# Kernel optimization log

Hardware: AMD Instinct MI355X
Metric: run time of the kernel (lower is better)

Reference implementation:

```python
import jax, jax.numpy as jnp
import numpy as np
import math

H = 16          # num_attention_heads
D = 64          # attention_head_size
MAX_POS = 1024  # max_position_embeddings


def setup_inputs() -> dict:
    key = jax.random.key(0)
    ks = jax.random.split(key, 6)
    B, S, HID = 4, 1024, 1024
    scale = 1.0 / math.sqrt(HID)
    return {
        "hidden_states": jax.random.normal(ks[0], (B, S, HID), jnp.float32),
        "attention_mask": jnp.zeros((B, 1, 1, S), jnp.float32),
        "Wq": jax.random.normal(ks[1], (HID, HID), jnp.float32) * scale,
        "bq": jnp.zeros((HID,), jnp.float32),
        "Wk": jax.random.normal(ks[2], (HID, HID), jnp.float32) * scale,
        "bk": jnp.zeros((HID,), jnp.float32),
        "Wv": jax.random.normal(ks[3], (HID, HID), jnp.float32) * scale,
        "bv": jnp.zeros((HID,), jnp.float32),
        "dist_emb": jax.random.normal(ks[4], (2 * MAX_POS - 1, D), jnp.float32) * 0.02,
    }


def _split_heads(x):
    # [B,S,H*D] -> [B,H,S,D]
    B, S, _ = x.shape
    return x.reshape(B, S, H, D).transpose(0, 2, 1, 3)


def reference(hidden_states, attention_mask, Wq, bq, Wk, bk, Wv, bv, dist_emb):
    B, S, _ = hidden_states.shape
    q = _split_heads(hidden_states @ Wq.T + bq)   # [B,H,S,D]
    k = _split_heads(hidden_states @ Wk.T + bk)
    v = _split_heads(hidden_states @ Wv.T + bv)

    scores = jnp.einsum("bhqd,bhkd->bhqk", q, k)  # [B,H,S,S]

    # relative_key_query positional bias
    pos_l = jnp.arange(S)[:, None]
    pos_r = jnp.arange(S)[None, :]
    distance = pos_l - pos_r + (MAX_POS - 1)      # [S,S] in [0, 2*MAX_POS-2]
    pos_emb = dist_emb[distance]                  # [S,S,D]
    rel_q = jnp.einsum("bhld,lrd->bhlr", q, pos_emb)
    rel_k = jnp.einsum("bhrd,lrd->bhlr", k, pos_emb)
    scores = (scores + rel_q + rel_k) / math.sqrt(D)

    scores = scores + attention_mask
    probs = jax.nn.softmax(scores, axis=-1)
    ctx = jnp.einsum("bhqk,bhkd->bhqd", probs, v)  # [B,H,S,D]
    ctx = ctx.transpose(0, 2, 1, 3).reshape(B, S, H * D)
    return ctx
```

## Files before the change

### kernel.cpp

```cpp
#include <hip/hip_runtime.h>
#include <hip/hip_bf16.h>

#define B_   4
#define S_   1024
#define HID_ 1024
#define H_   16
#define D_   64

typedef __attribute__((ext_vector_type(4))) float f32x4;
typedef __attribute__((ext_vector_type(8))) __bf16 bf16v8;
typedef __attribute__((ext_vector_type(8))) unsigned short u16x8;

#define MFMA16(a, b, c) __builtin_amdgcn_mfma_f32_16x16x32_bf16((a), (b), (c), 0, 0, 0)
#define GLOAD16(gp, lp)                                                              \
    __builtin_amdgcn_global_load_lds((const __attribute__((address_space(1))) void*)(gp), \
                                     (__attribute__((address_space(3))) void*)(lp), 16, 0, 0)

__device__ __forceinline__ unsigned short f2bs_hw(float f) {
    __bf16 h = (__bf16)f;
    return __builtin_bit_cast(unsigned short, h);
}
__device__ __forceinline__ unsigned pack2bf(float a, float b) {
    unsigned short lo = f2bs_hw(a), hi = f2bs_hw(b);
    return (unsigned)lo | ((unsigned)hi << 16);
}
__device__ __forceinline__ float bs2f(unsigned short s) {
    union { unsigned u; float f; } v; v.u = ((unsigned)s) << 16;
    return v.f;
}

__global__ void conv_kernel(const float* __restrict__ src, unsigned short* __restrict__ dst,
                            int n4) {
    int i = blockIdx.x * 256 + threadIdx.x;
    int stride = gridDim.x * 256;
    for (; i < n4; i += stride) {
        float4 x = *(const float4*)(src + (size_t)i * 4);
        uint2 o;
        o.x = pack2bf(x.x, x.y);
        o.y = pack2bf(x.z, x.w);
        *(uint2*)(dst + (size_t)i * 4) = o;
    }
}

__global__ __launch_bounds__(256)
void proj_kernel(const unsigned short* __restrict__ Xb,
                 const unsigned short* __restrict__ Wqb, const float* __restrict__ bq,
                 const unsigned short* __restrict__ Wkb, const float* __restrict__ bk,
                 const unsigned short* __restrict__ Wvb, const float* __restrict__ bv,
                 unsigned short* __restrict__ Qo, unsigned short* __restrict__ Ko,
                 unsigned short* __restrict__ Vo)
{
    __shared__ __align__(16) unsigned short Al[128][64];
    __shared__ __align__(16) unsigned short Bl[128][64];

    const int bid = blockIdx.x;
    const int tile = (bid & 7) * 96 + (bid >> 3);
    const int rt = tile / 24, ct = tile % 24;
    const int row0 = rt * 128, col0 = ct * 128;
    const int which = col0 >> 10;
    const unsigned short* Wm = (which == 0) ? Wqb : (which == 1) ? Wkb : Wvb;
    const float* bias        = (which == 0) ? bq  : (which == 1) ? bk  : bv;
    unsigned short* Out      = (which == 0) ? Qo  : (which == 1) ? Ko  : Vo;
    const int oc0 = col0 & 1023;

    const int t = threadIdx.x;
    const int lane = t & 63, w = t >> 6;
    const int wr = w >> 1, wc = w & 1;
    const int lg = lane >> 4, lc = lane & 15;

    f32x4 acc[4][4] = {};

    for (int k0 = 0; k0 < 1024; k0 += 64) {
        __syncthreads();
#pragma unroll
        for (int l = 0; l < 4; ++l) {
            int idx = l * 256 + t;
            int r = idx >> 3, su = idx & 7;
            int u = su ^ (r & 7);
            GLOAD16(Xb + (size_t)(row0 + r) * 1024 + k0 + u * 8,
                    &Al[0][0] + (size_t)(l * 256 + w * 64) * 8);
            GLOAD16(Wm + (size_t)(oc0 + r) * 1024 + k0 + u * 8,
                    &Bl[0][0] + (size_t)(l * 256 + w * 64) * 8);
        }
        __syncthreads();

        bf16v8 af[4][2], bfg[4][2];
#pragma unroll
        for (int m = 0; m < 4; ++m)
#pragma unroll
            for (int ks = 0; ks < 2; ++ks) {
                int u = (ks * 4 + lg) ^ (lc & 7);
                af[m][ks] = *(const bf16v8*)&Al[wr * 64 + m * 16 + lc][u * 8];
            }
#pragma unroll
        for (int n = 0; n < 4; ++n)
#pragma unroll
            for (int ks = 0; ks < 2; ++ks) {
                int u = (ks * 4 + lg) ^ (lc & 7);
                bfg[n][ks] = *(const bf16v8*)&Bl[wc * 64 + n * 16 + lc][u * 8];
            }
        __builtin_amdgcn_s_setprio(1);
#pragma unroll
        for (int m = 0; m < 4; ++m)
#pragma unroll
            for (int n = 0; n < 4; ++n) {
                acc[m][n] = MFMA16(af[m][0], bfg[n][0], acc[m][n]);
                acc[m][n] = MFMA16(af[m][1], bfg[n][1], acc[m][n]);
            }
        __builtin_amdgcn_s_setprio(0);
    }

#pragma unroll
    for (int m = 0; m < 4; ++m)
#pragma unroll
        for (int n = 0; n < 4; ++n) {
            int j = oc0 + wc * 64 + n * 16 + lc;
            int hh = j >> 6, dd = j & 63;
            float bv_ = bias[j];
#pragma unroll
            for (int r = 0; r < 4; ++r) {
                int i = row0 + wr * 64 + m * 16 + lg * 4 + r;
                int bb = i >> 10, ss = i & 1023;
                float v = acc[m][n][r] + bv_;
                Out[((size_t)(bb * 16 + hh) * 1024 + ss) * 64 + dd] = f2bs_hw(v);
            }
        }
}

__global__ __launch_bounds__(256)
void attn_kernel(const unsigned short* __restrict__ Q,
                 const unsigned short* __restrict__ K,
                 const unsigned short* __restrict__ V,
                 const float* __restrict__ mask,
                 const unsigned short* __restrict__ Eb,
                 float* __restrict__ Out)
{
    __shared__ __align__(16) unsigned short Kl[64][64];
    __shared__ __align__(16) unsigned short El[128][64];
    __shared__ __align__(16) unsigned short VTl[64][72];
    __shared__ __align__(16) unsigned short QDl[4][16][136];
    __shared__ __align__(16) unsigned short KDl[64][132];
    __shared__ __align__(16) unsigned Pex[4 * 16 * 36];
    __shared__ float maskl[64];

    const int t = threadIdx.x;
    const int lane = t & 63, w = t >> 6;
    const int lg = lane >> 4, lc = lane & 15;

    const int bid = blockIdx.x;
    const int bh = bid & 63;
    const int qt = bid >> 6;
    const int b = bh >> 4, h = bh & 15;
    const int i0 = qt * 64;
    const int i_loc = w * 16 + lc;

    const float C2 = 0.125f * 1.44269504089f;
    const float L2E = 1.44269504089f;

    const unsigned short* Qh = Q + (size_t)bh * S_ * D_;
    const unsigned short* Kh = K + (size_t)bh * S_ * D_;
    const unsigned short* Vh = V + (size_t)bh * S_ * D_;

    bf16v8 qf[2];
#pragma unroll
    for (int ks = 0; ks < 2; ++ks)
        qf[ks] = *(const bf16v8*)(Qh + (size_t)(i0 + i_loc) * D_ + ks * 32 + lg * 8);

    u16x8 ones_u;
#pragma unroll
    for (int e = 0; e < 8; ++e) ones_u[e] = 0x3F80;
    const bf16v8 onesf = __builtin_bit_cast(bf16v8, ones_u);

    float m_r = -1e30f;
    f32x4 lacc = (f32x4){0.f, 0.f, 0.f, 0.f};
    f32x4 ctx[4];
#pragma unroll
    for (int nd = 0; nd < 4; ++nd) ctx[nd] = (f32x4){0.f, 0.f, 0.f, 0.f};

    unsigned* PexW = &Pex[(w * 16 + lc) * 36];

    for (int jt = 0; jt < 16; ++jt) {
        const int j0 = jt * 64;
        const int dbase = i0 - j0 + 960;
        __syncthreads();

#pragma unroll
        for (int l = 0; l < 2; ++l) {
            int idx = l * 256 + t;
            int r = idx >> 3, su = idx & 7;
            int u = su ^ (r & 7);
            GLOAD16(Kh + (size_t)(j0 + r) * 64 + u * 8,
                    &Kl[0][0] + (size_t)(l * 256 + w * 64) * 8);
        }
        {
            int a = t & 7, rb = (t >> 3) << 1;
            int cq = a * 8;
            u16x8 v0 = *(const u16x8*)(Vh + (size_t)(j0 + rb) * 64 + cq);
            u16x8 v1 = *(const u16x8*)(Vh + (size_t)(j0 + rb + 1) * 64 + cq);
            int jst = (rb + (a << 3)) & 63;
#pragma unroll
            for (int e = 0; e < 8; ++e)
                *(unsigned*)&VTl[cq + e][jst] = (unsigned)v0[e] | ((unsigned)v1[e] << 16);
        }
        if (jt == 0) {
            const int sb0 = dbase & 127;
#pragma unroll
            for (int l = 0; l < 4; ++l) {
                int idx = l * 256 + t;
                int sl = idx >> 3, su = idx & 7;
                int u = su ^ (sl & 7);
                int dr = dbase + ((sl - sb0) & 127);
                if (dr > 2046) dr = 2046;
                GLOAD16(Eb + (size_t)dr * 64 + u * 8,
                        &El[0][0] + (size_t)(l * 256 + w * 64) * 8);
            }
        } else {
            const int sb = dbase & 127;
#pragma unroll
            for (int l = 0; l < 2; ++l) {
                int idx = l * 256 + t;
                int rl = idx >> 3, su = idx & 7;
                int u = su ^ (rl & 7);
                GLOAD16(Eb + (size_t)(dbase + rl) * 64 + u * 8,
                        &El[sb][0] + (size_t)(l * 256 + w * 64) * 8);
            }
        }
        if (t < 64) maskl[t] = mask[(size_t)b * S_ + j0 + t] * L2E;
        __syncthreads();

        bf16v8 kfa[2];
#pragma unroll
        for (int ks = 0; ks < 2; ++ks) {
            int u = (ks * 4 + lg) ^ (lc & 7);
            kfa[ks] = *(const bf16v8*)&Kl[w * 16 + lc][u * 8];
        }
        __builtin_amdgcn_s_setprio(1);
#pragma unroll
        for (int nd = 0; nd < 8; ++nd) {
            int sl = (dbase + nd * 16 + lc) & 127;
            int u0 = lg ^ (lc & 7);
            int u1 = (4 + lg) ^ (lc & 7);
            bf16v8 ef0 = *(const bf16v8*)&El[sl][u0 * 8];
            bf16v8 ef1 = *(const bf16v8*)&El[sl][u1 * 8];
            f32x4 kd = (f32x4){0.f, 0.f, 0.f, 0.f};
            kd = MFMA16(ef0, kfa[0], kd);
            kd = MFMA16(ef1, kfa[1], kd);
            uint2 pk;
            pk.x = pack2bf(kd[0], kd[1]);
            pk.y = pack2bf(kd[2], kd[3]);
            *(uint2*)&KDl[w * 16 + lc][nd * 16 + lg * 4] = pk;
            if (nd < 4 || jt == 0) {
                f32x4 qd = (f32x4){0.f, 0.f, 0.f, 0.f};
                qd = MFMA16(ef0, qf[0], qd);
                qd = MFMA16(ef1, qf[1], qd);
                int slot0 = ((dbase & 127) + nd * 16 + lg * 4) & 127;
                uint2 qk2;
                qk2.x = pack2bf(qd[0], qd[1]);
                qk2.y = pack2bf(qd[2], qd[3]);
                *(uint2*)&QDl[w][lc][slot0] = qk2;
            }
        }
        __builtin_amdgcn_s_setprio(0);
        __syncthreads();

        f32x4 s[4];
#pragma unroll
        for (int n = 0; n < 4; ++n) {
            s[n] = (f32x4){0.f, 0.f, 0.f, 0.f};
#pragma unroll
            for (int ks = 0; ks < 2; ++ks) {
                int u = (ks * 4 + lg) ^ (lc & 7);
                bf16v8 kb = *(const bf16v8*)&Kl[n * 16 + lc][u * 8];
                s[n] = MFMA16(kb, qf[ks], s[n]);
            }
        }

        const unsigned short* QDw = &QDl[w][lc][0];
        float vmax = -1e30f;
#pragma unroll
        for (int n = 0; n < 4; ++n) {
            int jb = n * 16 + lg * 4;
            float4 mk = *(const float4*)&maskl[jb];
            int kbase = jb * 131 + i_loc + 63;
            int qbase = dbase + i_loc - jb + 63;
#pragma unroll
            for (int r = 0; r < 4; ++r) {
                float qdv = bs2f(QDw[(qbase - r) & 127]);
                float kdv = bs2f((&KDl[0][0])[kbase + 131 * r]);
                float mkr = (r == 0) ? mk.x : (r == 1) ? mk.y : (r == 2) ? mk.z : mk.w;
                float val = (s[n][r] + qdv + kdv) * C2 + mkr;
                s[n][r] = val;
                vmax = fmaxf(vmax, val);
            }
        }
        vmax = fmaxf(vmax, __shfl_xor(vmax, 16));
        vmax = fmaxf(vmax, __shfl_xor(vmax, 32));

        if (__any(vmax > m_r)) {
            float mnew = fmaxf(m_r, vmax);
            float alpha = exp2f(m_r - mnew);
            m_r = mnew;
#pragma unroll
            for (int r = 0; r < 4; ++r) lacc[r] *= alpha;
#pragma unroll
            for (int nd = 0; nd < 4; ++nd)
#pragma unroll
                for (int r = 0; r < 4; ++r)
                    ctx[nd][r] *= alpha;
        }

#pragma unroll
        for (int n = 0; n < 4; ++n)
#pragma unroll
            for (int r = 0; r < 4; ++r)
                s[n][r] = exp2f(s[n][r] - m_r);

#pragma unroll
        for (int n = 0; n < 4; ++n) {
            uint2 pk;
            pk.x = pack2bf(s[n][0], s[n][1]);
            pk.y = pack2bf(s[n][2], s[n][3]);
            *(uint2*)&PexW[n * 8 + lg * 2] = pk;
        }
        bf16v8 pfB[2];
#pragma unroll
        for (int ks = 0; ks < 2; ++ks) {
            int nc = 2 * ks + (lg >> 1);
            pfB[ks] = *(const bf16v8*)&PexW[nc * 8 + (lg & 1) * 4];
        }

        __builtin_amdgcn_s_setprio(1);
        lacc = MFMA16(onesf, pfB[0], lacc);
        lacc = MFMA16(onesf, pfB[1], lacc);
#pragma unroll
        for (int nd = 0; nd < 4; ++nd) {
            int vrow = nd * 16 + lc;
#pragma unroll
            for (int ks = 0; ks < 2; ++ks) {
                int jst = (ks * 32 + lg * 8 + ((vrow >> 3) << 3)) & 63;
                bf16v8 vf = *(const bf16v8*)&VTl[vrow][jst];
                ctx[nd] = MFMA16(vf, pfB[ks], ctx[nd]);
            }
        }
        __builtin_amdgcn_s_setprio(0);
    }

    float inv = 1.0f / lacc[0];
    float* outp = Out + ((size_t)(b * S_ + i0 + i_loc) * H_ + h) * D_;
#pragma unroll
    for (int nd = 0; nd < 4; ++nd) {
        float4 o;
        o.x = ctx[nd][0] * inv;
        o.y = ctx[nd][1] * inv;
        o.z = ctx[nd][2] * inv;
        o.w = ctx[nd][3] * inv;
        *(float4*)(outp + nd * 16 + lg * 4) = o;
    }
}

extern "C" void kernel_launch(void* const* d_in, const int* in_sizes, int n_in,
                              void* d_out, int out_size, void* d_ws, size_t ws_size,
                              hipStream_t stream)
{
    const float* X    = (const float*)d_in[0];
    const float* mask = (const float*)d_in[1];
    const float* Wq   = (const float*)d_in[2];
    const float* bq   = (const float*)d_in[3];
    const float* Wk   = (const float*)d_in[4];
    const float* bk   = (const float*)d_in[5];
    const float* Wv   = (const float*)d_in[6];
    const float* bv   = (const float*)d_in[7];
    const float* E    = (const float*)d_in[8];
    float* Out = (float*)d_out;

    const size_t headN = (size_t)B_ * H_ * S_ * D_;
    unsigned short* Qw  = (unsigned short*)d_ws;
    unsigned short* Kw  = Qw + headN;
    unsigned short* Vw  = Kw + headN;
    unsigned short* Ebw = Vw + headN;
    unsigned short* Xb  = Ebw + (size_t)2047 * 64;
    unsigned short* Wqb = Xb + (size_t)4096 * 1024;
    unsigned short* Wkb = Wqb + (size_t)1024 * 1024;
    unsigned short* Wvb = Wkb + (size_t)1024 * 1024;

    conv_kernel<<<dim3(128),  dim3(256), 0, stream>>>(E,  Ebw, 2047 * 64 / 4);
    conv_kernel<<<dim3(2048), dim3(256), 0, stream>>>(X,  Xb,  4096 * 1024 / 4);
    conv_kernel<<<dim3(1024), dim3(256), 0, stream>>>(Wq, Wqb, 1024 * 1024 / 4);
    conv_kernel<<<dim3(1024), dim3(256), 0, stream>>>(Wk, Wkb, 1024 * 1024 / 4);
    conv_kernel<<<dim3(1024), dim3(256), 0, stream>>>(Wv, Wvb, 1024 * 1024 / 4);
    proj_kernel<<<dim3(768), dim3(256), 0, stream>>>(Xb, Wqb, bq, Wkb, bk, Wvb, bv, Qw, Kw, Vw);
    attn_kernel<<<dim3(1024), dim3(256), 0, stream>>>(Qw, Kw, Vw, mask, Ebw, Out);
}
```

Measured before the change: 167.6 us.

## Double-buffer projection GEMM, prefetch attention tiles, merge conversion launches

The projection GEMM now double-buffers its LDS tiles, so the next K-slice's global-to-LDS loads are issued while MFMAs run on the current slice, and one barrier per iteration is removed. The attention kernel prefetches the next K/E tiles, V registers and mask values after the score MFMAs, and computes the full QD bias each iteration into a per-row layout with simpler indexing. The four weight/embedding conversions are merged into one launch, and the X conversion uses one element per thread. The costs are twice the projection LDS, more attention registers, and extra QD MFMA work on every iteration.

```diff
diff --git a/kernel.cpp b/kernel.cpp
--- a/kernel.cpp
+++ b/kernel.cpp
@@ -32,8 +32,29 @@
 __global__ void conv_kernel(const float* __restrict__ src, unsigned short* __restrict__ dst,
                             int n4) {
     int i = blockIdx.x * 256 + threadIdx.x;
-    int stride = gridDim.x * 256;
-    for (; i < n4; i += stride) {
+    if (i < n4) {
+        float4 x = *(const float4*)(src + (size_t)i * 4);
+        uint2 o;
+        o.x = pack2bf(x.x, x.y);
+        o.y = pack2bf(x.z, x.w);
+        *(uint2*)(dst + (size_t)i * 4) = o;
+    }
+}
+
+__global__ void conv4_kernel(const float* __restrict__ Wq, const float* __restrict__ Wk,
+                             const float* __restrict__ Wv, const float* __restrict__ E,
+                             unsigned short* __restrict__ Wqb, unsigned short* __restrict__ Wkb,
+                             unsigned short* __restrict__ Wvb, unsigned short* __restrict__ Eb) {
+    int bid = blockIdx.x;
+    const float* src;
+    unsigned short* dst;
+    int n4, base;
+    if (bid < 1024)      { src = Wq; dst = Wqb; n4 = 262144; base = bid; }
+    else if (bid < 2048) { src = Wk; dst = Wkb; n4 = 262144; base = bid - 1024; }
+    else if (bid < 3072) { src = Wv; dst = Wvb; n4 = 262144; base = bid - 2048; }
+    else                 { src = E;  dst = Eb;  n4 = 32752;  base = bid - 3072; }
+    int i = base * 256 + threadIdx.x;
+    if (i < n4) {
         float4 x = *(const float4*)(src + (size_t)i * 4);
         uint2 o;
         o.x = pack2bf(x.x, x.y);
@@ -50,8 +71,8 @@
                  unsigned short* __restrict__ Qo, unsigned short* __restrict__ Ko,
                  unsigned short* __restrict__ Vo)
 {
-    __shared__ __align__(16) unsigned short Al[128][64];
-    __shared__ __align__(16) unsigned short Bl[128][64];
+    __shared__ __align__(16) unsigned short Al[2][128][64];
+    __shared__ __align__(16) unsigned short Bl[2][128][64];
 
     const int bid = blockIdx.x;
     const int tile = (bid & 7) * 96 + (bid >> 3);
@@ -70,34 +91,47 @@
 
     f32x4 acc[4][4] = {};
 
-    for (int k0 = 0; k0 < 1024; k0 += 64) {
+#pragma unroll
+    for (int l = 0; l < 4; ++l) {
+        int idx = l * 256 + t;
+        int r = idx >> 3, su = idx & 7;
+        int u = su ^ (r & 7);
+        GLOAD16(Xb + (size_t)(row0 + r) * 1024 + u * 8,
+                &Al[0][0][0] + (size_t)(l * 256 + w * 64) * 8);
+        GLOAD16(Wm + (size_t)(oc0 + r) * 1024 + u * 8,
+                &Bl[0][0][0] + (size_t)(l * 256 + w * 64) * 8);
+    }
+
+    for (int it = 0; it < 16; ++it) {
+        const int p = it & 1;
         __syncthreads();
-#pragma unroll
-        for (int l = 0; l < 4; ++l) {
-            int idx = l * 256 + t;
-            int r = idx >> 3, su = idx & 7;
-            int u = su ^ (r & 7);
-            GLOAD16(Xb + (size_t)(row0 + r) * 1024 + k0 + u * 8,
-                    &Al[0][0] + (size_t)(l * 256 + w * 64) * 8);
-            GLOAD16(Wm + (size_t)(oc0 + r) * 1024 + k0 + u * 8,
-                    &Bl[0][0] + (size_t)(l * 256 + w * 64) * 8);
-        }
-        __syncthreads();
-
+        if (it < 15) {
+            const int k1 = (it + 1) * 64;
+#pragma unroll
+            for (int l = 0; l < 4; ++l) {
+                int idx = l * 256 + t;
+                int r = idx >> 3, su = idx & 7;
+                int u = su ^ (r & 7);
+                GLOAD16(Xb + (size_t)(row0 + r) * 1024 + k1 + u * 8,
+                        &Al[p ^ 1][0][0] + (size_t)(l * 256 + w * 64) * 8);
+                GLOAD16(Wm + (size_t)(oc0 + r) * 1024 + k1 + u * 8,
+                        &Bl[p ^ 1][0][0] + (size_t)(l * 256 + w * 64) * 8);
+            }
+        }
         bf16v8 af[4][2], bfg[4][2];
 #pragma unroll
         for (int m = 0; m < 4; ++m)
 #pragma unroll
             for (int ks = 0; ks < 2; ++ks) {
                 int u = (ks * 4 + lg) ^ (lc & 7);
-                af[m][ks] = *(const bf16v8*)&Al[wr * 64 + m * 16 + lc][u * 8];
+                af[m][ks] = *(const bf16v8*)&Al[p][wr * 64 + m * 16 + lc][u * 8];
             }
 #pragma unroll
         for (int n = 0; n < 4; ++n)
 #pragma unroll
             for (int ks = 0; ks < 2; ++ks) {
                 int u = (ks * 4 + lg) ^ (lc & 7);
-                bfg[n][ks] = *(const bf16v8*)&Bl[wc * 64 + n * 16 + lc][u * 8];
+                bfg[n][ks] = *(const bf16v8*)&Bl[p][wc * 64 + n * 16 + lc][u * 8];
             }
         __builtin_amdgcn_s_setprio(1);
 #pragma unroll
@@ -138,8 +172,8 @@
     __shared__ __align__(16) unsigned short Kl[64][64];
     __shared__ __align__(16) unsigned short El[128][64];
     __shared__ __align__(16) unsigned short VTl[64][72];
-    __shared__ __align__(16) unsigned short QDl[4][16][136];
-    __shared__ __align__(16) unsigned short KDl[64][132];
+    __shared__ __align__(16) unsigned short QDl[64][134];
+    __shared__ __align__(16) unsigned short KDl[64][134];
     __shared__ __align__(16) unsigned Pex[4 * 16 * 36];
     __shared__ float maskl[64];
 
@@ -179,53 +213,50 @@
 
     unsigned* PexW = &Pex[(w * 16 + lc) * 36];
 
-    for (int jt = 0; jt < 16; ++jt) {
-        const int j0 = jt * 64;
-        const int dbase = i0 - j0 + 960;
-        __syncthreads();
-
+    const unsigned short* KD0 = &KDl[0][0] + lg * 4 * 133 + i_loc + 63;
+    const unsigned short* QD0 = &QDl[0][0] + i_loc * 135 + 12 - lg * 4;
+
+    const int va = t & 7, vrb = (t >> 3) << 1;
+    const int vcq = va * 8;
+    const int vjst = (vrb + (va << 3)) & 63;
+
+    u16x8 v0c, v1c;
+    float mkc;
+    {
 #pragma unroll
         for (int l = 0; l < 2; ++l) {
             int idx = l * 256 + t;
             int r = idx >> 3, su = idx & 7;
             int u = su ^ (r & 7);
-            GLOAD16(Kh + (size_t)(j0 + r) * 64 + u * 8,
+            GLOAD16(Kh + (size_t)r * 64 + u * 8,
                     &Kl[0][0] + (size_t)(l * 256 + w * 64) * 8);
         }
-        {
-            int a = t & 7, rb = (t >> 3) << 1;
-            int cq = a * 8;
-            u16x8 v0 = *(const u16x8*)(Vh + (size_t)(j0 + rb) * 64 + cq);
-            u16x8 v1 = *(const u16x8*)(Vh + (size_t)(j0 + rb + 1) * 64 + cq);
-            int jst = (rb + (a << 3)) & 63;
-#pragma unroll
-            for (int e = 0; e < 8; ++e)
-                *(unsigned*)&VTl[cq + e][jst] = (unsigned)v0[e] | ((unsigned)v1[e] << 16);
-        }
-        if (jt == 0) {
-            const int sb0 = dbase & 127;
-#pragma unroll
-            for (int l = 0; l < 4; ++l) {
-                int idx = l * 256 + t;
-                int sl = idx >> 3, su = idx & 7;
-                int u = su ^ (sl & 7);
-                int dr = dbase + ((sl - sb0) & 127);
-                if (dr > 2046) dr = 2046;
-                GLOAD16(Eb + (size_t)dr * 64 + u * 8,
-                        &El[0][0] + (size_t)(l * 256 + w * 64) * 8);
-            }
-        } else {
-            const int sb = dbase & 127;
-#pragma unroll
-            for (int l = 0; l < 2; ++l) {
-                int idx = l * 256 + t;
-                int rl = idx >> 3, su = idx & 7;
-                int u = su ^ (rl & 7);
-                GLOAD16(Eb + (size_t)(dbase + rl) * 64 + u * 8,
-                        &El[sb][0] + (size_t)(l * 256 + w * 64) * 8);
-            }
-        }
-        if (t < 64) maskl[t] = mask[(size_t)b * S_ + j0 + t] * L2E;
+        const int db0 = i0 + 960;
+        const int sb0 = db0 & 127;
+#pragma unroll
+        for (int l = 0; l < 4; ++l) {
+            int idx = l * 256 + t;
+            int sl = idx >> 3, su = idx & 7;
+            int u = su ^ (sl & 7);
+            int dr = db0 + ((sl - sb0) & 127);
+            if (dr > 2046) dr = 2046;
+            GLOAD16(Eb + (size_t)dr * 64 + u * 8,
+                    &El[0][0] + (size_t)(l * 256 + w * 64) * 8);
+        }
+        v0c = *(const u16x8*)(Vh + (size_t)vrb * 64 + vcq);
+        v1c = *(const u16x8*)(Vh + (size_t)(vrb + 1) * 64 + vcq);
+        mkc = (t < 64) ? mask[(size_t)b * S_ + t] * L2E : 0.f;
+    }
+
+    for (int jt = 0; jt < 16; ++jt) {
+        const int j0 = jt * 64;
+        const int dbase = i0 - j0 + 960;
+
+        __syncthreads();
+#pragma unroll
+        for (int e = 0; e < 8; ++e)
+            *(unsigned*)&VTl[vcq + e][vjst] = (unsigned)v0c[e] | ((unsigned)v1c[e] << 16);
+        if (t < 64) maskl[t] = mkc;
         __syncthreads();
 
         bf16v8 kfa[2];
@@ -234,10 +265,11 @@
             int u = (ks * 4 + lg) ^ (lc & 7);
             kfa[ks] = *(const bf16v8*)&Kl[w * 16 + lc][u * 8];
         }
+        const int slb = dbase + lc;
         __builtin_amdgcn_s_setprio(1);
 #pragma unroll
         for (int nd = 0; nd < 8; ++nd) {
-            int sl = (dbase + nd * 16 + lc) & 127;
+            int sl = (slb + nd * 16) & 127;
             int u0 = lg ^ (lc & 7);
             int u1 = (4 + lg) ^ (lc & 7);
             bf16v8 ef0 = *(const bf16v8*)&El[sl][u0 * 8];
@@ -249,20 +281,14 @@
             pk.x = pack2bf(kd[0], kd[1]);
             pk.y = pack2bf(kd[2], kd[3]);
             *(uint2*)&KDl[w * 16 + lc][nd * 16 + lg * 4] = pk;
-            if (nd < 4 || jt == 0) {
-                f32x4 qd = (f32x4){0.f, 0.f, 0.f, 0.f};
-                qd = MFMA16(ef0, qf[0], qd);
-                qd = MFMA16(ef1, qf[1], qd);
-                int slot0 = ((dbase & 127) + nd * 16 + lg * 4) & 127;
-                uint2 qk2;
-                qk2.x = pack2bf(qd[0], qd[1]);
-                qk2.y = pack2bf(qd[2], qd[3]);
-                *(uint2*)&QDl[w][lc][slot0] = qk2;
-            }
-        }
-        __builtin_amdgcn_s_setprio(0);
-        __syncthreads();
-
+            f32x4 qd = (f32x4){0.f, 0.f, 0.f, 0.f};
+            qd = MFMA16(ef0, qf[0], qd);
+            qd = MFMA16(ef1, qf[1], qd);
+            uint2 qk2;
+            qk2.x = pack2bf(qd[0], qd[1]);
+            qk2.y = pack2bf(qd[2], qd[3]);
+            *(uint2*)&QDl[w * 16 + lc][nd * 16 + lg * 4] = qk2;
+        }
         f32x4 s[4];
 #pragma unroll
         for (int n = 0; n < 4; ++n) {
@@ -274,20 +300,43 @@
                 s[n] = MFMA16(kb, qf[ks], s[n]);
             }
         }
-
-        const unsigned short* QDw = &QDl[w][lc][0];
+        __builtin_amdgcn_s_setprio(0);
+        __syncthreads();
+
+        if (jt < 15) {
+            const int j0n = j0 + 64;
+            const int dbn = dbase - 64;
+            const int sbn = dbn & 127;
+#pragma unroll
+            for (int l = 0; l < 2; ++l) {
+                int idx = l * 256 + t;
+                int r = idx >> 3, su = idx & 7;
+                int u = su ^ (r & 7);
+                GLOAD16(Kh + (size_t)(j0n + r) * 64 + u * 8,
+                        &Kl[0][0] + (size_t)(l * 256 + w * 64) * 8);
+            }
+#pragma unroll
+            for (int l = 0; l < 2; ++l) {
+                int idx = l * 256 + t;
+                int rl = idx >> 3, su = idx & 7;
+                int u = su ^ (rl & 7);
+                GLOAD16(Eb + (size_t)(dbn + rl) * 64 + u * 8,
+                        &El[sbn][0] + (size_t)(l * 256 + w * 64) * 8);
+            }
+            v0c = *(const u16x8*)(Vh + (size_t)(j0n + vrb) * 64 + vcq);
+            v1c = *(const u16x8*)(Vh + (size_t)(j0n + vrb + 1) * 64 + vcq);
+            mkc = (t < 64) ? mask[(size_t)b * S_ + j0n + t] * L2E : 0.f;
+        }
+
         float vmax = -1e30f;
 #pragma unroll
         for (int n = 0; n < 4; ++n) {
-            int jb = n * 16 + lg * 4;
-            float4 mk = *(const float4*)&maskl[jb];
-            int kbase = jb * 131 + i_loc + 63;
-            int qbase = dbase + i_loc - jb + 63;
+            float4 mk4 = *(const float4*)&maskl[n * 16 + lg * 4];
 #pragma unroll
             for (int r = 0; r < 4; ++r) {
-                float qdv = bs2f(QDw[(qbase - r) & 127]);
-                float kdv = bs2f((&KDl[0][0])[kbase + 131 * r]);
-                float mkr = (r == 0) ? mk.x : (r == 1) ? mk.y : (r == 2) ? mk.z : mk.w;
+                float qdv = bs2f(QD0[51 - 16 * n - r]);
+                float kdv = bs2f(KD0[133 * (16 * n + r)]);
+                float mkr = (r == 0) ? mk4.x : (r == 1) ? mk4.y : (r == 2) ? mk4.z : mk4.w;
                 float val = (s[n][r] + qdv + kdv) * C2 + mkr;
                 s[n][r] = val;
                 vmax = fmaxf(vmax, val);
@@ -383,11 +432,8 @@
     unsigned short* Wkb = Wqb + (size_t)1024 * 1024;
     unsigned short* Wvb = Wkb + (size_t)1024 * 1024;
 
-    conv_kernel<<<dim3(128),  dim3(256), 0, stream>>>(E,  Ebw, 2047 * 64 / 4);
-    conv_kernel<<<dim3(2048), dim3(256), 0, stream>>>(X,  Xb,  4096 * 1024 / 4);
-    conv_kernel<<<dim3(1024), dim3(256), 0, stream>>>(Wq, Wqb, 1024 * 1024 / 4);
-    conv_kernel<<<dim3(1024), dim3(256), 0, stream>>>(Wk, Wkb, 1024 * 1024 / 4);
-    conv_kernel<<<dim3(1024), dim3(256), 0, stream>>>(Wv, Wvb, 1024 * 1024 / 4);
+    conv_kernel<<<dim3(4096), dim3(256), 0, stream>>>(X, Xb, 4096 * 1024 / 4);
+    conv4_kernel<<<dim3(3200), dim3(256), 0, stream>>>(Wq, Wk, Wv, E, Wqb, Wkb, Wvb, Ebw);
     proj_kernel<<<dim3(768), dim3(256), 0, stream>>>(Xb, Wqb, bq, Wkb, bk, Wvb, bv, Qw, Kw, Vw);
     attn_kernel<<<dim3(1024), dim3(256), 0, stream>>>(Qw, Kw, Vw, mask, Ebw, Out);
 }
```

After: 173.5 us. 1.04x slower.

## Double-buffer projection GEMM tiles, merge conversion launches, move attn barrier

Applied to the files above, without the earlier changes.

The projection GEMM now double-buffers its LDS tiles, prefetching the next K-slice with global_load_lds while computing the current one, which removes one barrier per iteration. The four small weight/embedding conversion launches are merged into one kernel, and the X conversion uses one element per thread with no grid-stride loop. In the attention kernel a barrier and priority reset are moved after the QK score MFMAs so those overlap with other waves. The double buffer doubles LDS use in proj_kernel, which may lower occupancy.

```diff
diff --git a/kernel.cpp b/kernel.cpp
--- a/kernel.cpp
+++ b/kernel.cpp
@@ -10,6 +10,7 @@
 typedef __attribute__((ext_vector_type(4))) float f32x4;
 typedef __attribute__((ext_vector_type(8))) __bf16 bf16v8;
 typedef __attribute__((ext_vector_type(8))) unsigned short u16x8;
+typedef __attribute__((ext_vector_type(4))) unsigned short u16x4;
 
 #define MFMA16(a, b, c) __builtin_amdgcn_mfma_f32_16x16x32_bf16((a), (b), (c), 0, 0, 0)
 #define GLOAD16(gp, lp)                                                              \
@@ -32,8 +33,29 @@
 __global__ void conv_kernel(const float* __restrict__ src, unsigned short* __restrict__ dst,
                             int n4) {
     int i = blockIdx.x * 256 + threadIdx.x;
-    int stride = gridDim.x * 256;
-    for (; i < n4; i += stride) {
+    if (i < n4) {
+        float4 x = *(const float4*)(src + (size_t)i * 4);
+        uint2 o;
+        o.x = pack2bf(x.x, x.y);
+        o.y = pack2bf(x.z, x.w);
+        *(uint2*)(dst + (size_t)i * 4) = o;
+    }
+}
+
+__global__ void conv4_kernel(const float* __restrict__ Wq, const float* __restrict__ Wk,
+                             const float* __restrict__ Wv, const float* __restrict__ E,
+                             unsigned short* __restrict__ Wqb, unsigned short* __restrict__ Wkb,
+                             unsigned short* __restrict__ Wvb, unsigned short* __restrict__ Eb) {
+    int bid = blockIdx.x;
+    const float* src;
+    unsigned short* dst;
+    int n4, base;
+    if (bid < 1024)      { src = Wq; dst = Wqb; n4 = 262144; base = bid; }
+    else if (bid < 2048) { src = Wk; dst = Wkb; n4 = 262144; base = bid - 1024; }
+    else if (bid < 3072) { src = Wv; dst = Wvb; n4 = 262144; base = bid - 2048; }
+    else                 { src = E;  dst = Eb;  n4 = 32752;  base = bid - 3072; }
+    int i = base * 256 + threadIdx.x;
+    if (i < n4) {
         float4 x = *(const float4*)(src + (size_t)i * 4);
         uint2 o;
         o.x = pack2bf(x.x, x.y);
@@ -50,8 +72,8 @@
                  unsigned short* __restrict__ Qo, unsigned short* __restrict__ Ko,
                  unsigned short* __restrict__ Vo)
 {
-    __shared__ __align__(16) unsigned short Al[128][64];
-    __shared__ __align__(16) unsigned short Bl[128][64];
+    __shared__ __align__(16) unsigned short Al[2][128][64];
+    __shared__ __align__(16) unsigned short Bl[2][128][64];
 
     const int bid = blockIdx.x;
     const int tile = (bid & 7) * 96 + (bid >> 3);
@@ -70,34 +92,47 @@
 
     f32x4 acc[4][4] = {};
 
-    for (int k0 = 0; k0 < 1024; k0 += 64) {
+#pragma unroll
+    for (int l = 0; l < 4; ++l) {
+        int idx = l * 256 + t;
+        int r = idx >> 3, su = idx & 7;
+        int u = su ^ (r & 7);
+        GLOAD16(Xb + (size_t)(row0 + r) * 1024 + u * 8,
+                &Al[0][0][0] + (size_t)(l * 256 + w * 64) * 8);
+        GLOAD16(Wm + (size_t)(oc0 + r) * 1024 + u * 8,
+                &Bl[0][0][0] + (size_t)(l * 256 + w * 64) * 8);
+    }
+
+    for (int it = 0; it < 16; ++it) {
+        const int p = it & 1;
         __syncthreads();
-#pragma unroll
-        for (int l = 0; l < 4; ++l) {
-            int idx = l * 256 + t;
-            int r = idx >> 3, su = idx & 7;
-            int u = su ^ (r & 7);
-            GLOAD16(Xb + (size_t)(row0 + r) * 1024 + k0 + u * 8,
-                    &Al[0][0] + (size_t)(l * 256 + w * 64) * 8);
-            GLOAD16(Wm + (size_t)(oc0 + r) * 1024 + k0 + u * 8,
-                    &Bl[0][0] + (size_t)(l * 256 + w * 64) * 8);
-        }
-        __syncthreads();
-
+        if (it < 15) {
+            const int k1 = (it + 1) * 64;
+#pragma unroll
+            for (int l = 0; l < 4; ++l) {
+                int idx = l * 256 + t;
+                int r = idx >> 3, su = idx & 7;
+                int u = su ^ (r & 7);
+                GLOAD16(Xb + (size_t)(row0 + r) * 1024 + k1 + u * 8,
+                        &Al[p ^ 1][0][0] + (size_t)(l * 256 + w * 64) * 8);
+                GLOAD16(Wm + (size_t)(oc0 + r) * 1024 + k1 + u * 8,
+                        &Bl[p ^ 1][0][0] + (size_t)(l * 256 + w * 64) * 8);
+            }
+        }
         bf16v8 af[4][2], bfg[4][2];
 #pragma unroll
         for (int m = 0; m < 4; ++m)
 #pragma unroll
             for (int ks = 0; ks < 2; ++ks) {
                 int u = (ks * 4 + lg) ^ (lc & 7);
-                af[m][ks] = *(const bf16v8*)&Al[wr * 64 + m * 16 + lc][u * 8];
+                af[m][ks] = *(const bf16v8*)&Al[p][wr * 64 + m * 16 + lc][u * 8];
             }
 #pragma unroll
         for (int n = 0; n < 4; ++n)
 #pragma unroll
             for (int ks = 0; ks < 2; ++ks) {
                 int u = (ks * 4 + lg) ^ (lc & 7);
-                bfg[n][ks] = *(const bf16v8*)&Bl[wc * 64 + n * 16 + lc][u * 8];
+                bfg[n][ks] = *(const bf16v8*)&Bl[p][wc * 64 + n * 16 + lc][u * 8];
             }
         __builtin_amdgcn_s_setprio(1);
 #pragma unroll
@@ -260,9 +295,6 @@
                 *(uint2*)&QDl[w][lc][slot0] = qk2;
             }
         }
-        __builtin_amdgcn_s_setprio(0);
-        __syncthreads();
-
         f32x4 s[4];
 #pragma unroll
         for (int n = 0; n < 4; ++n) {
@@ -274,6 +306,8 @@
                 s[n] = MFMA16(kb, qf[ks], s[n]);
             }
         }
+        __builtin_amdgcn_s_setprio(0);
+        __syncthreads();
 
         const unsigned short* QDw = &QDl[w][lc][0];
         float vmax = -1e30f;
@@ -383,11 +417,8 @@
     unsigned short* Wkb = Wqb + (size_t)1024 * 1024;
     unsigned short* Wvb = Wkb + (size_t)1024 * 1024;
 
-    conv_kernel<<<dim3(128),  dim3(256), 0, stream>>>(E,  Ebw, 2047 * 64 / 4);
-    conv_kernel<<<dim3(2048), dim3(256), 0, stream>>>(X,  Xb,  4096 * 1024 / 4);
-    conv_kernel<<<dim3(1024), dim3(256), 0, stream>>>(Wq, Wqb, 1024 * 1024 / 4);
-    conv_kernel<<<dim3(1024), dim3(256), 0, stream>>>(Wk, Wkb, 1024 * 1024 / 4);
-    conv_kernel<<<dim3(1024), dim3(256), 0, stream>>>(Wv, Wvb, 1024 * 1024 / 4);
+    conv_kernel<<<dim3(4096), dim3(256), 0, stream>>>(X, Xb, 4096 * 1024 / 4);
+    conv4_kernel<<<dim3(3200), dim3(256), 0, stream>>>(Wq, Wk, Wv, E, Wqb, Wkb, Wvb, Ebw);
     proj_kernel<<<dim3(768), dim3(256), 0, stream>>>(Xb, Wqb, bq, Wkb, bk, Wvb, bv, Qw, Kw, Vw);
     attn_kernel<<<dim3(1024), dim3(256), 0, stream>>>(Qw, Kw, Vw, mask, Ebw, Out);
 }
```

Result: faster. 153.8 us (-8.2%).
